# Performance work log

Hardware: AMD Instinct MI355X
Metric: run time of the kernel (lower is better)

## Reference

```python
import jax, jax.numpy as jnp
import numpy as np

B, T, D = 8, 2048, 512
KQ, K = 32, 4  # DemandRouter defaults: k_query=32, k_topk=4


def setup_inputs() -> dict:
    key = jax.random.key(0)
    ks = jax.random.split(key, 9)

    def init(k, shape, fan_in):
        return (jax.random.normal(k, shape, jnp.float32) / np.sqrt(fan_in)).astype(jnp.float32)

    return dict(
        x=jax.random.normal(ks[0], (B, T, D), jnp.float32),
        # DemandRouter projections
        Wq=init(ks[1], (D, KQ), D), bq=jnp.zeros((KQ,), jnp.float32),
        Wk=init(ks[2], (D, KQ), D), bk=jnp.zeros((KQ,), jnp.float32),
        # System1 FFN (D -> 2D -> D) + LayerNorm
        W1=init(ks[3], (D, 2 * D), D), b1=jnp.zeros((2 * D,), jnp.float32),
        W2=init(ks[4], (2 * D, D), 2 * D), b2=jnp.zeros((D,), jnp.float32),
        ln_g=jnp.ones((D,), jnp.float32), ln_b=jnp.zeros((D,), jnp.float32),
        # System2 transform (2D -> 2D -> D)
        Wt1=init(ks[5], (2 * D, 2 * D), 2 * D), bt1=jnp.zeros((2 * D,), jnp.float32),
        Wt2=init(ks[6], (2 * D, D), 2 * D), bt2=jnp.zeros((D,), jnp.float32),
        # output projection
        Wo=init(ks[7], (D, D), D), bo=jnp.zeros((D,), jnp.float32),
    )


def reference(x, Wq, bq, Wk, bk, W1, b1, W2, b2, ln_g, ln_b, Wt1, bt1, Wt2, bt2, Wo, bo):
    # ---- DemandRouter: topk over query-key similarity, gather neighbors, mean ----
    q = x @ Wq + bq                      # [B,T,KQ]
    k = x @ Wk + bk                      # [B,T,KQ]
    sim = jnp.einsum('btk,bsk->bts', q, k) / np.float32(np.sqrt(KQ))  # [B,T,T]
    _, idx = jax.lax.top_k(sim, K)       # [B,T,K]
    # gather x[b, idx[b,t]] and mean over K neighbors -> [B,T,D]
    gathered = jax.vmap(lambda xb, ib: xb[ib])(x, idx).mean(axis=2)

    # ---- System1: residual FFN (exact GELU) + LayerNorm ----
    h = jax.nn.gelu(gathered @ W1 + b1, approximate=False) @ W2 + b2
    y = gathered + h
    mu = y.mean(-1, keepdims=True)
    var = y.var(-1, keepdims=True)
    y = (y - mu) / jnp.sqrt(var + 1e-5) * ln_g + ln_b  # [B,T,D]

    # ---- System2: sequential gated memory update over T ----
    def step(mem, xt):  # mem: [B,D], xt: [B,D]
        e = jnp.concatenate([xt, mem], axis=-1)                       # [B,2D]
        prop = jax.nn.gelu(e @ Wt1 + bt1, approximate=False) @ Wt2 + bt2  # [B,D]
        g = jax.nn.sigmoid(prop)
        mem = mem * (1.0 - g) + prop * g
        return mem, None

    mem0 = jnp.zeros((y.shape[0], y.shape[2]), y.dtype)
    mem_final, _ = jax.lax.scan(step, mem0, jnp.swapaxes(y, 0, 1))

    # pooled = system2_out[:, -1] == final memory
    return mem_final @ Wo + bo  # [B,D]
```

## Files before the change

### kernel.cpp

```cpp
#include <hip/hip_runtime.h>
#include <math.h>
#include <stdint.h>


using bf16x8 = __attribute__((ext_vector_type(8))) short;
using f32x4v = __attribute__((ext_vector_type(4))) float;
typedef unsigned long long ull;

__device__ inline unsigned short f2b(float f) {
  union { float f; unsigned int u; } v; v.f = f;
  unsigned int r = v.u + 0x7fffu + ((v.u >> 16) & 1u);
  return (unsigned short)(r >> 16);
}

__device__ inline float gelu_f(float x) {
  return 0.5f * x * (1.0f + erff(x * 0.70710678118654752f));
}

__device__ inline void ins4(float v, int i,
                            float& v0, int& i0, float& v1, int& i1,
                            float& v2, int& i2, float& v3, int& i3) {
  bool b0 = (v > v0) || (v == v0 && i < i0);
  bool b1 = (v > v1) || (v == v1 && i < i1);
  bool b2 = (v > v2) || (v == v2 && i < i2);
  bool b3 = (v > v3) || (v == v3 && i < i3);
  float nv3 = b2 ? v2 : (b3 ? v : v3); int ni3 = b2 ? i2 : (b3 ? i : i3);
  float nv2 = b1 ? v1 : (b2 ? v : v2); int ni2 = b1 ? i1 : (b2 ? i : i2);
  float nv1 = b0 ? v0 : (b1 ? v : v1); int ni1 = b0 ? i0 : (b1 ? i : i1);
  float nv0 = b0 ? v  : v0;            int ni0 = b0 ? i  : i0;
  v0=nv0; i0=ni0; v1=nv1; i1=ni1; v2=nv2; i2=ni2; v3=nv3; i3=ni3;
}


__global__ __launch_bounds__(256)
void wqk_kernel(const float* __restrict__ Wq, const float* __restrict__ Wk,
                float* __restrict__ wqk) {
  int id = blockIdx.x * 256 + threadIdx.x;
  int d = id >> 6, c = id & 63;
  wqk[id] = (c < 32) ? Wq[d * 32 + c] : Wk[d * 32 + (c - 32)];
}

__global__ __launch_bounds__(256)
void transpose_bf16_kernel(const float* __restrict__ src,
                           unsigned short* __restrict__ dst, int K, int N) {
  __shared__ float tile[32][33];
  int bk = blockIdx.x << 5, bn = blockIdx.y << 5;
  int c = threadIdx.x & 31, r8 = threadIdx.x >> 5;
  for (int r = r8; r < 32; r += 8) tile[r][c] = src[(size_t)(bk + r) * N + bn + c];
  __syncthreads();
  for (int r = r8; r < 32; r += 8) dst[(size_t)(bn + r) * K + bk + c] = f2b(tile[c][r]);
}


__global__ __launch_bounds__(256)
void qk_kernel(const float* __restrict__ x, const float* __restrict__ wqk,
               const float* __restrict__ bq, const float* __restrict__ bk,
               float* __restrict__ qkout) {
  __shared__ float xs[16][512];
  int tid = threadIdx.x;
  int b = blockIdx.x >> 7;
  int t0 = (blockIdx.x & 127) << 4;
  const float* xb = x + ((size_t)(b * 2048 + t0)) * 512;
#pragma unroll
  for (int i = 0; i < 8; ++i) {
    int f = i * 256 + tid;
    int r = f >> 7, c4 = f & 127;
    *(float4*)&xs[r][c4 * 4] = *(const float4*)&xb[(size_t)r * 512 + c4 * 4];
  }
  __syncthreads();
  int c = tid & 63, r4 = tid >> 6;
  float a0 = 0.f, a1 = 0.f, a2 = 0.f, a3 = 0.f;
#pragma unroll 4
  for (int d = 0; d < 512; ++d) {
    float w = wqk[d * 64 + c];
    a0 += xs[r4][d] * w;
    a1 += xs[r4 + 4][d] * w;
    a2 += xs[r4 + 8][d] * w;
    a3 += xs[r4 + 12][d] * w;
  }
  float bias = (c < 32) ? bq[c] : bk[c - 32];
  size_t base = ((size_t)(b * 2048 + t0)) * 64 + c;
  qkout[base + (size_t)r4 * 64] = a0 + bias;
  qkout[base + (size_t)(r4 + 4) * 64] = a1 + bias;
  qkout[base + (size_t)(r4 + 8) * 64] = a2 + bias;
  qkout[base + (size_t)(r4 + 12) * 64] = a3 + bias;
}

__global__ __launch_bounds__(256)
void topk_kernel(const float* __restrict__ qkb, int* __restrict__ idxout) {
  __shared__ float qs[16][36];
  __shared__ float ks[128][36];
  __shared__ float mv[16][16][4];
  __shared__ int   mi[16][16][4];
  int tid = threadIdx.x;
  int b = blockIdx.x >> 7;
  int t0 = (blockIdx.x & 127) << 4;
  const float* qb = qkb + ((size_t)b * 2048) * 64;
  if (tid < 128) {
    int r = tid >> 3, c4 = tid & 7;
    *(float4*)&qs[r][c4 * 4] = *(const float4*)&qb[(size_t)(t0 + r) * 64 + c4 * 4];
  }
  __syncthreads();
  int tl = tid >> 4, sl = tid & 15;
  float qv[32];
#pragma unroll
  for (int kk = 0; kk < 32; ++kk) qv[kk] = qs[tl][kk];
  float v0 = -INFINITY, v1 = -INFINITY, v2 = -INFINITY, v3 = -INFINITY;
  int i0 = 0x7fffffff, i1 = 0x7fffffff, i2 = 0x7fffffff, i3 = 0x7fffffff;
  for (int s0 = 0; s0 < 2048; s0 += 128) {
    __syncthreads();
#pragma unroll
    for (int p = 0; p < 4; ++p) {
      int f = p * 256 + tid;
      int r = f >> 3, c4 = f & 7;
      *(float4*)&ks[r][c4 * 4] =
          *(const float4*)&qb[(size_t)(s0 + r) * 64 + 32 + c4 * 4];
    }
    __syncthreads();
#pragma unroll
    for (int j = 0; j < 8; ++j) {
      int srow = j * 16 + sl;
      float accv = 0.f;
#pragma unroll
      for (int k4 = 0; k4 < 8; ++k4) {
        float4 kv = *(const float4*)&ks[srow][k4 * 4];
        accv += qv[k4 * 4 + 0] * kv.x + qv[k4 * 4 + 1] * kv.y +
                qv[k4 * 4 + 2] * kv.z + qv[k4 * 4 + 3] * kv.w;
      }
      ins4(accv, s0 + srow, v0, i0, v1, i1, v2, i2, v3, i3);
    }
  }
  mv[tl][sl][0] = v0; mv[tl][sl][1] = v1; mv[tl][sl][2] = v2; mv[tl][sl][3] = v3;
  mi[tl][sl][0] = i0; mi[tl][sl][1] = i1; mi[tl][sl][2] = i2; mi[tl][sl][3] = i3;
  __syncthreads();
  if (tid < 16) {
    float w0 = -INFINITY, w1 = -INFINITY, w2 = -INFINITY, w3 = -INFINITY;
    int a0 = 0x7fffffff, a1 = 0x7fffffff, a2 = 0x7fffffff, a3 = 0x7fffffff;
    for (int ss = 0; ss < 16; ++ss)
#pragma unroll
      for (int q = 0; q < 4; ++q)
        ins4(mv[tid][ss][q], mi[tid][ss][q], w0, a0, w1, a1, w2, a2, w3, a3);
    int4 o; o.x = a0; o.y = a1; o.z = a2; o.w = a3;
    *(int4*)&idxout[((size_t)(b * 2048 + t0 + tid)) * 4] = o;
  }
}

__global__ __launch_bounds__(128)
void gather_kernel(const float* __restrict__ x, const int* __restrict__ idx,
                   float* __restrict__ gf, unsigned short* __restrict__ gb) {
  int bt = blockIdx.x;
  int b = bt >> 11;
  const int4 iv = *(const int4*)&idx[(size_t)bt * 4];
  int tid = threadIdx.x;
  const float* xb = x + ((size_t)b * 2048) * 512;
  float4 p0 = *(const float4*)&xb[(size_t)iv.x * 512 + tid * 4];
  float4 p1 = *(const float4*)&xb[(size_t)iv.y * 512 + tid * 4];
  float4 p2 = *(const float4*)&xb[(size_t)iv.z * 512 + tid * 4];
  float4 p3 = *(const float4*)&xb[(size_t)iv.w * 512 + tid * 4];
  float4 m;
  m.x = (p0.x + p1.x + p2.x + p3.x) * 0.25f;
  m.y = (p0.y + p1.y + p2.y + p3.y) * 0.25f;
  m.z = (p0.z + p1.z + p2.z + p3.z) * 0.25f;
  m.w = (p0.w + p1.w + p2.w + p3.w) * 0.25f;
  *(float4*)&gf[(size_t)bt * 512 + tid * 4] = m;
  ushort4 u; u.x = f2b(m.x); u.y = f2b(m.y); u.z = f2b(m.z); u.w = f2b(m.w);
  *(ushort4*)&gb[(size_t)bt * 512 + tid * 4] = u;
}


template <int MODE>
__global__ __launch_bounds__(256, 2)
void gemm_bf16_k(const unsigned short* __restrict__ A,
                 const unsigned short* __restrict__ Bt,
                 const float* __restrict__ bias,
                 const float* __restrict__ resid,
                 void* __restrict__ outp, int M, int N, int K) {
  __shared__ unsigned short sA[128 * 32];
  __shared__ unsigned short sB[128 * 32];
  const int tid = threadIdx.x;
  const int lane = tid & 63, wave = tid >> 6;
  const int m0 = blockIdx.x * 128, n0 = blockIdx.y * 128;
  const int col16 = lane & 15, quad = lane >> 4;
  const int wm = wave >> 1, wn = wave & 1;
  f32x4v acc[4][4];
#pragma unroll
  for (int i = 0; i < 4; ++i)
#pragma unroll
    for (int j = 0; j < 4; ++j) {
      f32x4v z = {0.f, 0.f, 0.f, 0.f};
      acc[i][j] = z;
    }
  const int nkt = K >> 5;
  for (int kt = 0; kt < nkt; ++kt) {
    const int k0 = kt << 5;
#pragma unroll
    for (int p = 0; p < 2; ++p) {
      int f = p * 256 + tid;
      int row = f >> 2, q4 = f & 3;
      *(uint4*)&sA[row * 32 + q4 * 8] =
          *(const uint4*)(A + (size_t)(m0 + row) * K + k0 + q4 * 8);
      *(uint4*)&sB[row * 32 + q4 * 8] =
          *(const uint4*)(Bt + (size_t)(n0 + row) * K + k0 + q4 * 8);
    }
    __syncthreads();
    bf16x8 af[4], bfr[4];
#pragma unroll
    for (int i = 0; i < 4; ++i)
      af[i] = *(const bf16x8*)&sA[(wm * 64 + i * 16 + col16) * 32 + quad * 8];
#pragma unroll
    for (int j = 0; j < 4; ++j)
      bfr[j] = *(const bf16x8*)&sB[(wn * 64 + j * 16 + col16) * 32 + quad * 8];
#pragma unroll
    for (int i = 0; i < 4; ++i)
#pragma unroll
      for (int j = 0; j < 4; ++j)
        acc[i][j] = __builtin_amdgcn_mfma_f32_16x16x32_bf16(af[i], bfr[j],
                                                            acc[i][j], 0, 0, 0);
    __syncthreads();
  }
  float* outf = (float*)outp;
  unsigned short* outb = (unsigned short*)outp;
#pragma unroll
  for (int i = 0; i < 4; ++i)
#pragma unroll
    for (int j = 0; j < 4; ++j) {
      int col = n0 + wn * 64 + j * 16 + col16;
      float bs = bias[col];
#pragma unroll
      for (int r = 0; r < 4; ++r) {
        int row = m0 + wm * 64 + i * 16 + quad * 4 + r;
        float v = acc[i][j][r] + bs;
        if (MODE == 0) {
          outb[(size_t)row * N + col] = f2b(gelu_f(v));
        } else if (MODE == 1) {
          outf[(size_t)row * N + col] = v + resid[(size_t)row * N + col];
        } else {
          outf[(size_t)row * N + col] = v;
        }
      }
    }
}


__global__ __launch_bounds__(128)
void ln_kernel(const float* __restrict__ ypre, const float* __restrict__ lg,
               const float* __restrict__ lb, unsigned short* __restrict__ yb) {
  int row = blockIdx.x, tid = threadIdx.x;
  float4 v = *(const float4*)&ypre[(size_t)row * 512 + tid * 4];
  float s = v.x + v.y + v.z + v.w;
  float sq = v.x * v.x + v.y * v.y + v.z * v.z + v.w * v.w;
#pragma unroll
  for (int off = 1; off < 64; off <<= 1) {
    s += __shfl_xor(s, off, 64);
    sq += __shfl_xor(sq, off, 64);
  }
  __shared__ float red[4];
  if ((tid & 63) == 0) { red[(tid >> 6) * 2] = s; red[(tid >> 6) * 2 + 1] = sq; }
  __syncthreads();
  float S = red[0] + red[2], SQ = red[1] + red[3];
  float mu = S * (1.f / 512.f);
  float var = SQ * (1.f / 512.f) - mu * mu;
  float rstd = rsqrtf(var + 1e-5f);
  float4 g4 = *(const float4*)&lg[tid * 4];
  float4 b4 = *(const float4*)&lb[tid * 4];
  ushort4 u;
  u.x = f2b((v.x - mu) * rstd * g4.x + b4.x);
  u.y = f2b((v.y - mu) * rstd * g4.y + b4.y);
  u.z = f2b((v.z - mu) * rstd * g4.z + b4.z);
  u.w = f2b((v.w - mu) * rstd * g4.w + b4.w);
  *(ushort4*)&yb[(size_t)row * 512 + tid * 4] = u;
}


__global__ __launch_bounds__(256)
void system2_kernel(const float* __restrict__ Wt1, const float* __restrict__ Wt2,
                    const float* __restrict__ bt2, const float* __restrict__ xpart,
                    float* __restrict__ slotbuf, float* __restrict__ membuf,
                    int* __restrict__ flagA, int* __restrict__ flagB,
                    float* __restrict__ memfinal) {
  __shared__ float WbT[32 * 516];
  __shared__ float WtS[32 * 512];
  __shared__ float memS[512];
  __shared__ float parts1[256];
  __shared__ float red2[256];
  __shared__ float guL[32];

  const int t = threadIdx.x;
  const int team = blockIdx.x & 7;
  const int g = blockIdx.x >> 3;
  const int ucol0 = g << 5;
  const int mcol0 = g << 4;

  for (int idx = t; idx < 32 * 512; idx += 256) {
    int j = idx & 31, k = idx >> 5;
    WbT[j * 516 + k] = Wt1[(size_t)(512 + k) * 1024 + ucol0 + j];
  }
  for (int idx = t; idx < 32 * 512; idx += 256) {
    int u = idx >> 9, d = idx & 511;
    WtS[u * 512 + d] = Wt2[(size_t)(ucol0 + u) * 512 + d];
  }
  memS[t] = 0.f;
  memS[t + 256] = 0.f;
  const float bt2r = (t < 16) ? bt2[mcol0 + t] : 0.f;
  __syncthreads();

  const int j = t & 31, c = t >> 5;
  const float* xp = xpart + (size_t)team * 2048 * 1024 + ucol0;
  float xv = (t < 32) ? xp[t] : 0.f;

  for (int s = 0; s < 2048; ++s) {
    const int par = s & 1;
    float* slot = slotbuf + ((size_t)(par * 8 + team) * 32) * 512;
    float* memb = membuf + (size_t)(par * 8 + team) * 512;
    int* flA = flagA + (par * 8 + team) * 32;
    int* flB = flagB + (par * 8 + team) * 32;
    const int tag = s + 1;

    float xnext = (t < 32 && s < 2047) ? xp[(size_t)(s + 1) * 1024 + t] : 0.f;

    {
      const float* wrow = &WbT[j * 516 + c * 64];
      const float* mrow = &memS[c * 64];
      float p1 = 0.f;
#pragma unroll
      for (int i = 0; i < 64; i += 4) {
        float4 wv = *(const float4*)&wrow[i];
        float4 mv = *(const float4*)&mrow[i];
        p1 += wv.x * mv.x + wv.y * mv.y + wv.z * mv.z + wv.w * mv.w;
      }
      parts1[c * 32 + j] = p1;
    }
    __syncthreads();
    if (t < 32) {
      float u = xv;
#pragma unroll
      for (int cc = 0; cc < 8; ++cc) u += parts1[cc * 32 + t];
      guL[t] = gelu_f(u);
    }
    __syncthreads();

    {
      const int d2 = t << 1;
      float px = 0.f, py = 0.f;
#pragma unroll
      for (int u = 0; u < 32; ++u) {
        float gv = guL[u];
        float2 wv = *(const float2*)&WtS[u * 512 + d2];
        px += gv * wv.x;
        py += gv * wv.y;
      }
      union { float2 f2; ull u64; } cv;
      cv.f2 = make_float2(px, py);
      __hip_atomic_store((ull*)&slot[g * 512 + d2], cv.u64, __ATOMIC_RELAXED,
                         __HIP_MEMORY_SCOPE_AGENT);
    }
    __syncthreads();
    if (t == 0)
      __hip_atomic_store(&flA[g], tag, __ATOMIC_RELAXED,
                         __HIP_MEMORY_SCOPE_AGENT);
    if (t < 64) {
      int f = (t < 32) ? 0 : tag;
      const int* fp = &flA[t < 32 ? t : 0];
      while (true) {
        if (t < 32 && f != tag)
          f = __hip_atomic_load(fp, __ATOMIC_RELAXED, __HIP_MEMORY_SCOPE_AGENT);
        if (__ballot(f == tag) == ~0ull) break;
        __builtin_amdgcn_s_sleep(1);
      }
    }
    __syncthreads();
    __builtin_amdgcn_fence(__ATOMIC_ACQUIRE, "workgroup");

    {
      const int w = t >> 4, dd = t & 15;
      float v1 = __hip_atomic_load(&slot[w * 512 + mcol0 + dd], __ATOMIC_RELAXED,
                                   __HIP_MEMORY_SCOPE_AGENT);
      float v2 = __hip_atomic_load(&slot[(w + 16) * 512 + mcol0 + dd],
                                   __ATOMIC_RELAXED, __HIP_MEMORY_SCOPE_AGENT);
      red2[w * 16 + dd] = v1 + v2;
    }
    __syncthreads();
    if (t < 16) {
      float prop = bt2r;
#pragma unroll
      for (int w = 0; w < 16; ++w) prop += red2[w * 16 + t];
      float gate = 1.f / (1.f + __expf(-prop));
      float mnew = memS[mcol0 + t] * (1.f - gate) + prop * gate;
      __hip_atomic_store(&memb[mcol0 + t], mnew, __ATOMIC_RELAXED,
                         __HIP_MEMORY_SCOPE_AGENT);
    }
    __syncthreads();
    if (t == 0)
      __hip_atomic_store(&flB[g], tag, __ATOMIC_RELAXED,
                         __HIP_MEMORY_SCOPE_AGENT);
    if (t < 64) {
      int f = (t < 32) ? 0 : tag;
      const int* fp = &flB[t < 32 ? t : 0];
      while (true) {
        if (t < 32 && f != tag)
          f = __hip_atomic_load(fp, __ATOMIC_RELAXED, __HIP_MEMORY_SCOPE_AGENT);
        if (__ballot(f == tag) == ~0ull) break;
        __builtin_amdgcn_s_sleep(1);
      }
    }
    __syncthreads();
    __builtin_amdgcn_fence(__ATOMIC_ACQUIRE, "workgroup");

    if (t < 128) {
      union { float2 f2; ull u64; } a, b;
      a.u64 = __hip_atomic_load((ull*)&memb[t * 4], __ATOMIC_RELAXED,
                                __HIP_MEMORY_SCOPE_AGENT);
      b.u64 = __hip_atomic_load((ull*)&memb[t * 4 + 2], __ATOMIC_RELAXED,
                                __HIP_MEMORY_SCOPE_AGENT);
      memS[t * 4 + 0] = a.f2.x;
      memS[t * 4 + 1] = a.f2.y;
      memS[t * 4 + 2] = b.f2.x;
      memS[t * 4 + 3] = b.f2.y;
    }
    xv = xnext;
    __syncthreads();
  }

  if (g == 0 && t < 128)
    *(float4*)&memfinal[(size_t)team * 512 + t * 4] = *(float4*)&memS[t * 4];
}


__global__ __launch_bounds__(256)
void out_gemv_kernel(const float* __restrict__ memf, const float* __restrict__ Wo,
                     const float* __restrict__ bo, float* __restrict__ out) {
  int gid = blockIdx.x * 256 + threadIdx.x;
  int b = gid >> 9, d = gid & 511;
  const float* mb = memf + (size_t)b * 512;
  float acc = bo[d];
#pragma unroll 8
  for (int k = 0; k < 512; ++k) acc += mb[k] * Wo[(size_t)k * 512 + d];
  out[gid] = acc;
}


extern "C" void kernel_launch(void* const* d_in, const int* in_sizes, int n_in,
                              void* d_out, int out_size, void* d_ws, size_t ws_size,
                              hipStream_t stream) {
  const float* x   = (const float*)d_in[0];
  const float* Wq  = (const float*)d_in[1];
  const float* bq  = (const float*)d_in[2];
  const float* Wk  = (const float*)d_in[3];
  const float* bk  = (const float*)d_in[4];
  const float* W1  = (const float*)d_in[5];
  const float* b1  = (const float*)d_in[6];
  const float* W2  = (const float*)d_in[7];
  const float* b2  = (const float*)d_in[8];
  const float* lng = (const float*)d_in[9];
  const float* lnb = (const float*)d_in[10];
  const float* Wt1 = (const float*)d_in[11];
  const float* bt1 = (const float*)d_in[12];
  const float* Wt2 = (const float*)d_in[13];
  const float* bt2 = (const float*)d_in[14];
  const float* Wo  = (const float*)d_in[15];
  const float* bo  = (const float*)d_in[16];
  float* out = (float*)d_out;

  char* ws = (char*)d_ws;
  size_t off = 0;
  auto alloc = [&](size_t bytes) -> void* {
    void* p = ws + off;
    off += (bytes + 255) & ~(size_t)255;
    return p;
  };
  float* qk             = (float*)alloc(8ull * 2048 * 64 * 4);
  int* idxb             = (int*)alloc(8ull * 2048 * 4 * 4);
  float* gathf          = (float*)alloc(16384ull * 512 * 4);
  unsigned short* gathb = (unsigned short*)alloc(16384ull * 512 * 2);
  unsigned short* h1b   = (unsigned short*)alloc(16384ull * 1024 * 2);
  float* ypre           = (float*)alloc(16384ull * 512 * 4);
  unsigned short* yb    = (unsigned short*)alloc(16384ull * 512 * 2);
  float* xpart          = (float*)alloc(16384ull * 1024 * 4);
  unsigned short* w1t   = (unsigned short*)alloc(1024ull * 512 * 2);
  unsigned short* w2t   = (unsigned short*)alloc(512ull * 1024 * 2);
  unsigned short* wt1t  = (unsigned short*)alloc(1024ull * 512 * 2);
  float* wqkb           = (float*)alloc(512ull * 64 * 4);
  float* slotbuf        = (float*)alloc(2ull * 8 * 32 * 512 * 4);
  float* membuf         = (float*)alloc(2ull * 8 * 512 * 4);
  int* flagA            = (int*)alloc(2ull * 8 * 32 * 4);
  int* flagB            = (int*)alloc(2ull * 8 * 32 * 4);
  float* memf           = (float*)alloc(8ull * 512 * 4);
  if (off > ws_size) return;

  wqk_kernel<<<128, 256, 0, stream>>>(Wq, Wk, wqkb);
  transpose_bf16_kernel<<<dim3(16, 32), 256, 0, stream>>>(W1, w1t, 512, 1024);
  transpose_bf16_kernel<<<dim3(32, 16), 256, 0, stream>>>(W2, w2t, 1024, 512);
  transpose_bf16_kernel<<<dim3(16, 32), 256, 0, stream>>>(Wt1, wt1t, 512, 1024);

  qk_kernel<<<1024, 256, 0, stream>>>(x, wqkb, bq, bk, qk);
  topk_kernel<<<1024, 256, 0, stream>>>(qk, idxb);
  gather_kernel<<<16384, 128, 0, stream>>>(x, idxb, gathf, gathb);

  gemm_bf16_k<0><<<dim3(128, 8), 256, 0, stream>>>(gathb, w1t, b1, nullptr, h1b,
                                                   16384, 1024, 512);
  gemm_bf16_k<1><<<dim3(128, 4), 256, 0, stream>>>(h1b, w2t, b2, gathf, ypre,
                                                   16384, 512, 1024);
  ln_kernel<<<16384, 128, 0, stream>>>(ypre, lng, lnb, yb);
  gemm_bf16_k<2><<<dim3(128, 8), 256, 0, stream>>>(yb, wt1t, bt1, nullptr, xpart,
                                                   16384, 1024, 512);

  system2_kernel<<<256, 256, 0, stream>>>(Wt1, Wt2, bt2, xpart, slotbuf, membuf,
                                          flagA, flagB, memf);
  out_gemv_kernel<<<16, 256, 0, stream>>>(memf, Wo, bo, out);
}
```

Before: 7.996 ms.

## Exchange GELU activations with tagged 64-bit words instead of partial sums and flags

The sequential System2 scan now broadcasts each block's 32 GELU activations to all peers as 64-bit words that pack a step tag with the value. Each block then computes its own 16 output columns from the full 1024-wide activation vector, using a re-sliced Wt2 held in shared memory. This removes the separate flag barriers and the cross-block partial-sum reduction. Memory updates use the same tagged-word scheme, so each step needs two data-carrying exchanges rather than two flag waits plus data reads. The cost is more redundant per-block work on Wt2 (1024x16 per block) and spin-polling on many global words.

```diff
diff --git a/kernel.cpp b/kernel.cpp
--- a/kernel.cpp
+++ b/kernel.cpp
@@ -275,15 +275,14 @@
 __global__ __launch_bounds__(256)
 void system2_kernel(const float* __restrict__ Wt1, const float* __restrict__ Wt2,
                     const float* __restrict__ bt2, const float* __restrict__ xpart,
-                    float* __restrict__ slotbuf, float* __restrict__ membuf,
-                    int* __restrict__ flagA, int* __restrict__ flagB,
+                    ull* __restrict__ gubuf, ull* __restrict__ membuf,
                     float* __restrict__ memfinal) {
   __shared__ float WbT[32 * 516];
-  __shared__ float WtS[32 * 512];
+  __shared__ float Wt2S[1024 * 16];
+  __shared__ float guS[1024];
   __shared__ float memS[512];
   __shared__ float parts1[256];
   __shared__ float red2[256];
-  __shared__ float guL[32];
 
   const int t = threadIdx.x;
   const int team = blockIdx.x & 7;
@@ -295,9 +294,9 @@
     int j = idx & 31, k = idx >> 5;
     WbT[j * 516 + k] = Wt1[(size_t)(512 + k) * 1024 + ucol0 + j];
   }
-  for (int idx = t; idx < 32 * 512; idx += 256) {
-    int u = idx >> 9, d = idx & 511;
-    WtS[u * 512 + d] = Wt2[(size_t)(ucol0 + u) * 512 + d];
+  for (int idx = t; idx < 1024 * 16; idx += 256) {
+    int u = idx >> 4, dd = idx & 15;
+    Wt2S[u * 16 + dd] = Wt2[(size_t)u * 512 + mcol0 + dd];
   }
   memS[t] = 0.f;
   memS[t + 256] = 0.f;
@@ -305,16 +304,16 @@
   __syncthreads();
 
   const int j = t & 31, c = t >> 5;
+  const int w = t >> 4, dd = t & 15;
+  const bool skipown = (t >> 3) == g;
   const float* xp = xpart + (size_t)team * 2048 * 1024 + ucol0;
   float xv = (t < 32) ? xp[t] : 0.f;
 
   for (int s = 0; s < 2048; ++s) {
     const int par = s & 1;
-    float* slot = slotbuf + ((size_t)(par * 8 + team) * 32) * 512;
-    float* memb = membuf + (size_t)(par * 8 + team) * 512;
-    int* flA = flagA + (par * 8 + team) * 32;
-    int* flB = flagB + (par * 8 + team) * 32;
-    const int tag = s + 1;
+    ull* gub = gubuf + (size_t)(par * 8 + team) * 1024;
+    ull* memb = membuf + (size_t)(par * 8 + team) * 512;
+    const ull tagv = (ull)(unsigned)(s + 1) << 32;
 
     float xnext = (t < 32 && s < 2047) ? xp[(size_t)(s + 1) * 1024 + t] : 0.f;
 
@@ -335,87 +334,73 @@
       float u = xv;
 #pragma unroll
       for (int cc = 0; cc < 8; ++cc) u += parts1[cc * 32 + t];
-      guL[t] = gelu_f(u);
+      float gv = gelu_f(u);
+      guS[ucol0 + t] = gv;
+      union { float f; unsigned u32; } cv; cv.f = gv;
+      __hip_atomic_store(&gub[ucol0 + t], tagv | cv.u32, __ATOMIC_RELAXED,
+                         __HIP_MEMORY_SCOPE_AGENT);
+    }
+    if (!skipown) {
+      const int u4 = t << 2;
+      ull v0, v1, v2, v3;
+      while (true) {
+        v0 = __hip_atomic_load(&gub[u4 + 0], __ATOMIC_RELAXED,
+                               __HIP_MEMORY_SCOPE_AGENT);
+        v1 = __hip_atomic_load(&gub[u4 + 1], __ATOMIC_RELAXED,
+                               __HIP_MEMORY_SCOPE_AGENT);
+        v2 = __hip_atomic_load(&gub[u4 + 2], __ATOMIC_RELAXED,
+                               __HIP_MEMORY_SCOPE_AGENT);
+        v3 = __hip_atomic_load(&gub[u4 + 3], __ATOMIC_RELAXED,
+                               __HIP_MEMORY_SCOPE_AGENT);
+        bool ok = ((v0 >> 32) == (tagv >> 32)) && ((v1 >> 32) == (tagv >> 32)) &&
+                  ((v2 >> 32) == (tagv >> 32)) && ((v3 >> 32) == (tagv >> 32));
+        if (ok) break;
+        __builtin_amdgcn_s_sleep(1);
+      }
+      union { unsigned u32; float f; } a;
+      a.u32 = (unsigned)v0; guS[u4 + 0] = a.f;
+      a.u32 = (unsigned)v1; guS[u4 + 1] = a.f;
+      a.u32 = (unsigned)v2; guS[u4 + 2] = a.f;
+      a.u32 = (unsigned)v3; guS[u4 + 3] = a.f;
     }
     __syncthreads();
 
     {
-      const int d2 = t << 1;
-      float px = 0.f, py = 0.f;
-#pragma unroll
-      for (int u = 0; u < 32; ++u) {
-        float gv = guL[u];
-        float2 wv = *(const float2*)&WtS[u * 512 + d2];
-        px += gv * wv.x;
-        py += gv * wv.y;
-      }
-      union { float2 f2; ull u64; } cv;
-      cv.f2 = make_float2(px, py);
-      __hip_atomic_store((ull*)&slot[g * 512 + d2], cv.u64, __ATOMIC_RELAXED,
-                         __HIP_MEMORY_SCOPE_AGENT);
-    }
-    __syncthreads();
-    if (t == 0)
-      __hip_atomic_store(&flA[g], tag, __ATOMIC_RELAXED,
-                         __HIP_MEMORY_SCOPE_AGENT);
-    if (t < 64) {
-      int f = (t < 32) ? 0 : tag;
-      const int* fp = &flA[t < 32 ? t : 0];
-      while (true) {
-        if (t < 32 && f != tag)
-          f = __hip_atomic_load(fp, __ATOMIC_RELAXED, __HIP_MEMORY_SCOPE_AGENT);
-        if (__ballot(f == tag) == ~0ull) break;
-        __builtin_amdgcn_s_sleep(1);
-      }
-    }
-    __syncthreads();
-    __builtin_amdgcn_fence(__ATOMIC_ACQUIRE, "workgroup");
-
-    {
-      const int w = t >> 4, dd = t & 15;
-      float v1 = __hip_atomic_load(&slot[w * 512 + mcol0 + dd], __ATOMIC_RELAXED,
-                                   __HIP_MEMORY_SCOPE_AGENT);
-      float v2 = __hip_atomic_load(&slot[(w + 16) * 512 + mcol0 + dd],
-                                   __ATOMIC_RELAXED, __HIP_MEMORY_SCOPE_AGENT);
-      red2[w * 16 + dd] = v1 + v2;
+      float p2 = 0.f;
+#pragma unroll
+      for (int i = 0; i < 64; ++i) {
+        const int u = i * 16 + w;
+        p2 += guS[u] * Wt2S[u * 16 + dd];
+      }
+      red2[w * 16 + dd] = p2;
     }
     __syncthreads();
     if (t < 16) {
       float prop = bt2r;
 #pragma unroll
-      for (int w = 0; w < 16; ++w) prop += red2[w * 16 + t];
+      for (int ww = 0; ww < 16; ++ww) prop += red2[ww * 16 + t];
       float gate = 1.f / (1.f + __expf(-prop));
       float mnew = memS[mcol0 + t] * (1.f - gate) + prop * gate;
-      __hip_atomic_store(&memb[mcol0 + t], mnew, __ATOMIC_RELAXED,
+      memS[mcol0 + t] = mnew;
+      union { float f; unsigned u32; } cv; cv.f = mnew;
+      __hip_atomic_store(&memb[mcol0 + t], tagv | cv.u32, __ATOMIC_RELAXED,
                          __HIP_MEMORY_SCOPE_AGENT);
     }
-    __syncthreads();
-    if (t == 0)
-      __hip_atomic_store(&flB[g], tag, __ATOMIC_RELAXED,
-                         __HIP_MEMORY_SCOPE_AGENT);
-    if (t < 64) {
-      int f = (t < 32) ? 0 : tag;
-      const int* fp = &flB[t < 32 ? t : 0];
+    if (!skipown) {
+      const int d2 = t << 1;
+      ull v0, v1;
       while (true) {
-        if (t < 32 && f != tag)
-          f = __hip_atomic_load(fp, __ATOMIC_RELAXED, __HIP_MEMORY_SCOPE_AGENT);
-        if (__ballot(f == tag) == ~0ull) break;
+        v0 = __hip_atomic_load(&memb[d2 + 0], __ATOMIC_RELAXED,
+                               __HIP_MEMORY_SCOPE_AGENT);
+        v1 = __hip_atomic_load(&memb[d2 + 1], __ATOMIC_RELAXED,
+                               __HIP_MEMORY_SCOPE_AGENT);
+        bool ok = ((v0 >> 32) == (tagv >> 32)) && ((v1 >> 32) == (tagv >> 32));
+        if (ok) break;
         __builtin_amdgcn_s_sleep(1);
       }
-    }
-    __syncthreads();
-    __builtin_amdgcn_fence(__ATOMIC_ACQUIRE, "workgroup");
-
-    if (t < 128) {
-      union { float2 f2; ull u64; } a, b;
-      a.u64 = __hip_atomic_load((ull*)&memb[t * 4], __ATOMIC_RELAXED,
-                                __HIP_MEMORY_SCOPE_AGENT);
-      b.u64 = __hip_atomic_load((ull*)&memb[t * 4 + 2], __ATOMIC_RELAXED,
-                                __HIP_MEMORY_SCOPE_AGENT);
-      memS[t * 4 + 0] = a.f2.x;
-      memS[t * 4 + 1] = a.f2.y;
-      memS[t * 4 + 2] = b.f2.x;
-      memS[t * 4 + 3] = b.f2.y;
+      union { unsigned u32; float f; } a;
+      a.u32 = (unsigned)v0; memS[d2 + 0] = a.f;
+      a.u32 = (unsigned)v1; memS[d2 + 1] = a.f;
     }
     xv = xnext;
     __syncthreads();
@@ -480,10 +465,8 @@
   unsigned short* w2t   = (unsigned short*)alloc(512ull * 1024 * 2);
   unsigned short* wt1t  = (unsigned short*)alloc(1024ull * 512 * 2);
   float* wqkb           = (float*)alloc(512ull * 64 * 4);
-  float* slotbuf        = (float*)alloc(2ull * 8 * 32 * 512 * 4);
-  float* membuf         = (float*)alloc(2ull * 8 * 512 * 4);
-  int* flagA            = (int*)alloc(2ull * 8 * 32 * 4);
-  int* flagB            = (int*)alloc(2ull * 8 * 32 * 4);
+  ull* gubuf            = (ull*)alloc(2ull * 8 * 1024 * 8);
+  ull* membuf           = (ull*)alloc(2ull * 8 * 512 * 8);
   float* memf           = (float*)alloc(8ull * 512 * 4);
   if (off > ws_size) return;
 
@@ -504,7 +487,7 @@
   gemm_bf16_k<2><<<dim3(128, 8), 256, 0, stream>>>(yb, wt1t, bt1, nullptr, xpart,
                                                    16384, 1024, 512);
 
-  system2_kernel<<<256, 256, 0, stream>>>(Wt1, Wt2, bt2, xpart, slotbuf, membuf,
-                                          flagA, flagB, memf);
+  system2_kernel<<<256, 256, 0, stream>>>(Wt1, Wt2, bt2, xpart, gubuf, membuf,
+                                          memf);
   out_gemv_kernel<<<16, 256, 0, stream>>>(memf, Wo, bo, out);
 }
```

New measurement: 9.694 ms. 1.21x slower.
